# Kernel tuning notes

Measured on AMD Instinct MI355X. Metric: run time of the kernel, lower is better.

## Reference

```python
import jax, jax.numpy as jnp
import numpy as np

B, T, NT, H, L, F, NH, R = 2, 1024, 30, 1024, 8, 2816, 16, 16
HD = H // NH
LORA_SCALE = 32.0 / 16.0  # lora_alpha / r
CLAMP = 10.0
EPS = 1e-6


def _rms(x, w):
    return x * jax.lax.rsqrt(jnp.mean(x * x, axis=-1, keepdims=True) + EPS) * w


def _rope(x):
    # x: [B,T,NH,HD] -- LLaMA rotary embedding
    half = HD // 2
    inv_freq = 1.0 / (10000.0 ** (jnp.arange(0, half, dtype=jnp.float32) / half))
    ang = jnp.arange(x.shape[1], dtype=jnp.float32)[:, None] * inv_freq  # [T,half]
    cos = jnp.concatenate([jnp.cos(ang), jnp.cos(ang)], -1)[None, :, None, :]
    sin = jnp.concatenate([jnp.sin(ang), jnp.sin(ang)], -1)[None, :, None, :]
    x1, x2 = x[..., :half], x[..., half:]
    return x * cos + jnp.concatenate([-x2, x1], -1) * sin


def _lora(x, W, A, Bm):
    # W: [in,out], A: [r,in], Bm: [out,r]  (dequantized base + LoRA update)
    return x @ W + ((x @ A.T) @ Bm.T) * LORA_SCALE


def setup_inputs():
    key = jax.random.key(0)
    ks = jax.random.split(key, 16)
    n = lambda k, s, sc=0.02: jax.random.normal(k, s, jnp.float32) * sc
    return {
        'x': jax.random.normal(ks[0], (B, T, NT), jnp.float32),
        'temperature': jnp.float32(1.0),
        'state_W': n(ks[1], (NT, H), 0.1),
        'state_b': jnp.zeros((H,), jnp.float32),
        'ln1': jnp.ones((L, H), jnp.float32),
        'ln2': jnp.ones((L, H), jnp.float32),
        'Wqkv': n(ks[2], (L, 3, H, H)),
        'Aqkv': n(ks[3], (L, 3, R, H)),
        'Bqkv': n(ks[4], (L, 3, H, R)),
        'Wo': n(ks[5], (L, H, H)),
        'Ao': n(ks[6], (L, R, H)),
        'Bo': n(ks[7], (L, H, R)),
        'Wgu': n(ks[8], (L, 2, H, F)),
        'Agu': n(ks[9], (L, 2, R, H)),
        'Bgu': n(ks[10], (L, 2, F, R)),
        'Wd': n(ks[11], (L, F, H)),
        'Ad': n(ks[12], (L, R, F)),
        'Bd': n(ks[13], (L, H, R)),
        'ln_f': jnp.ones((H,), jnp.float32),
        'head_W': n(ks[14], (H, NT + 1), 0.01),
        'head_b': jnp.zeros((NT + 1,), jnp.float32),
    }


def reference(x, temperature, state_W, state_b, ln1, ln2, Wqkv, Aqkv, Bqkv,
              Wo, Ao, Bo, Wgu, Agu, Bgu, Wd, Ad, Bd, ln_f, head_W, head_b):
    causal = jnp.tril(jnp.ones((T, T), bool))

    def layer(h, p):
        l1, l2, wqkv, aqkv, bqkv, wo, ao, bo, wgu, agu, bgu, wd, ad, bd = p
        hn = _rms(h, l1)
        qkv = jnp.einsum('bth,khd->kbtd', hn, wqkv)
        qkv = qkv + jnp.einsum('kbtr,kdr->kbtd',
                               jnp.einsum('bth,krh->kbtr', hn, aqkv), bqkv) * LORA_SCALE
        q = _rope(qkv[0].reshape(B, T, NH, HD))
        k = _rope(qkv[1].reshape(B, T, NH, HD))
        v = qkv[2].reshape(B, T, NH, HD)
        scores = jnp.einsum('bqhd,bkhd->bhqk', q, k) / np.sqrt(HD).astype(np.float32)
        scores = jnp.where(causal, scores, jnp.float32(-1e9))
        probs = jax.nn.softmax(scores, axis=-1)
        att = jnp.einsum('bhqk,bkhd->bqhd', probs, v).reshape(B, T, H)
        h = h + _lora(att, wo, ao, bo)
        hn2 = _rms(h, l2)
        gu = jnp.einsum('bth,khf->kbtf', hn2, wgu)
        gu = gu + jnp.einsum('kbtr,kfr->kbtf',
                             jnp.einsum('bth,krh->kbtr', hn2, agu), bgu) * LORA_SCALE
        act = jax.nn.silu(gu[0]) * gu[1]
        h = h + _lora(act, wd, ad, bd)
        return h, None

    h = x @ state_W + state_b  # state encoder -> inputs_embeds
    h, _ = jax.lax.scan(layer, h, (ln1, ln2, Wqkv, Aqkv, Bqkv, Wo, Ao, Bo,
                                   Wgu, Agu, Bgu, Wd, Ad, Bd))
    latent = _rms(h, ln_f)  # last hidden state
    logits = latent @ head_W + head_b
    logits_clamped = jnp.clip(logits, -CLAMP, CLAMP)
    portfolio_weights = jax.nn.softmax(logits_clamped / temperature, axis=-1)
    return portfolio_weights, logits_clamped
```

## Files before the change

### kernel.cpp

```cpp
#include <hip/hip_runtime.h>
#include <hip/hip_bf16.h>
#include <cstdint>

#define B_    2
#define T_    1024
#define NT_   30
#define H_    1024
#define L_    8
#define F_    2816
#define NH_   16
#define R_    16
#define HD_   64
#define M_    2048
#define NTP1_ 31

typedef unsigned short u16;
typedef short  s16x8 __attribute__((ext_vector_type(8)));
typedef unsigned short u16x4 __attribute__((ext_vector_type(4)));
typedef unsigned short u16x8 __attribute__((ext_vector_type(8)));
typedef float  f32x4 __attribute__((ext_vector_type(4)));

__device__ __forceinline__ u16 f2bf(float f){
  __hip_bfloat16 h = __float2bfloat16(f);
  return __builtin_bit_cast(unsigned short, h);
}
__device__ __forceinline__ float bf2f(u16 u){
  uint32_t v = (uint32_t)u << 16;
  return __builtin_bit_cast(float, v);
}

__device__ __forceinline__ void async16(const void* g, void* l){
  __builtin_amdgcn_global_load_lds((const __attribute__((address_space(1))) void*)g,
                                   (__attribute__((address_space(3))) void*)l, 16, 0, 0);
}

__global__ __launch_bounds__(256, 3) void fold_kernel(
    const float* __restrict__ W, const float* __restrict__ A,
    const float* __restrict__ Bm, u16* __restrict__ Wt,
    int K, int N, long strW, long strA, long strB, long strWt)
{
  const int mat = blockIdx.z;
  W  += (long)mat * strW;  A  += (long)mat * strA;
  Bm += (long)mat * strB;  Wt += (long)mat * strWt;
  const int k0 = blockIdx.x * 64, n0 = blockIdx.y * 64;
  __shared__ float Wt_s[64][65];
  __shared__ float As[16][64];
  __shared__ float Bs[64][20];
  const int tid = threadIdx.x;
  {
    const int kr = tid >> 4;
    const int n4 = (tid & 15) * 4;
    #pragma unroll
    for (int p = 0; p < 4; p++){
      int krow = p * 16 + kr;
      float4 w = *(const float4*)(W + (long)(k0 + krow) * N + n0 + n4);
      Wt_s[n4+0][krow] = w.x; Wt_s[n4+1][krow] = w.y;
      Wt_s[n4+2][krow] = w.z; Wt_s[n4+3][krow] = w.w;
    }
    const int r = tid >> 4, kc = (tid & 15) * 4;
    *(float4*)&As[r][kc] = *(const float4*)(A + (long)r * K + k0 + kc);
    const int nb = tid >> 2, r4 = (tid & 3) * 4;
    float4 b = *(const float4*)(Bm + (long)(n0 + nb) * 16 + r4);
    Bs[nb][r4+0]=b.x; Bs[nb][r4+1]=b.y; Bs[nb][r4+2]=b.z; Bs[nb][r4+3]=b.w;
  }
  __syncthreads();
  const int ko = (tid & 7) * 8;
  const int na = tid >> 3;
  float bq0[16], bq1[16];
  #pragma unroll
  for (int c = 0; c < 4; c++){
    *(float4*)&bq0[c*4] = *(const float4*)&Bs[na][c*4];
    *(float4*)&bq1[c*4] = *(const float4*)&Bs[na+32][c*4];
  }
  float l0[8] = {}, l1[8] = {};
  #pragma unroll
  for (int r = 0; r < 16; r++){
    float a[8];
    *(float4*)&a[0] = *(const float4*)&As[r][ko];
    *(float4*)&a[4] = *(const float4*)&As[r][ko+4];
    #pragma unroll
    for (int j = 0; j < 8; j++){
      l0[j] += a[j] * bq0[r];
      l1[j] += a[j] * bq1[r];
    }
  }
  u16x8 o0, o1;
  #pragma unroll
  for (int j = 0; j < 8; j++){
    o0[j] = f2bf(Wt_s[na][ko+j]    + 2.0f * l0[j]);
    o1[j] = f2bf(Wt_s[na+32][ko+j] + 2.0f * l1[j]);
  }
  *(u16x8*)(Wt + (long)(n0+na)*K    + k0 + ko) = o0;
  *(u16x8*)(Wt + (long)(n0+na+32)*K + k0 + ko) = o1;
}

__global__ __launch_bounds__(256) void embed_kernel(
    const float* __restrict__ x, const float* __restrict__ sw,
    const float* __restrict__ sb, float* __restrict__ h)
{
  const int m = blockIdx.x;
  const float* xr = x + (long)m * NT_;
  for (int jj = threadIdx.x; jj < H_; jj += 256){
    float acc = sb[jj];
    #pragma unroll
    for (int i = 0; i < NT_; i++) acc += xr[i] * sw[i * H_ + jj];
    h[(long)m * H_ + jj] = acc;
  }
}

__global__ __launch_bounds__(256) void rms_kernel(
    float* __restrict__ hsrc, const float* __restrict__ pb,
    const float* __restrict__ w, u16* __restrict__ outp, int nparts)
{
  const int m = blockIdx.x, t = threadIdx.x;
  float4 v = ((const float4*)(hsrc + (long)m * H_))[t];
  if (nparts){
    for (int k = 0; k < nparts; k++){
      const float4 a = ((const float4*)(pb + (long)k * M_ * H_ + (long)m * H_))[t];
      v.x += a.x; v.y += a.y; v.z += a.z; v.w += a.w;
    }
    ((float4*)(hsrc + (long)m * H_))[t] = v;
  }
  float ss = v.x*v.x + v.y*v.y + v.z*v.z + v.w*v.w;
  #pragma unroll
  for (int off = 32; off >= 1; off >>= 1) ss += __shfl_xor(ss, off);
  __shared__ float red[4];
  if ((t & 63) == 0) red[t >> 6] = ss;
  __syncthreads();
  const float scale = rsqrtf((red[0]+red[1]+red[2]+red[3]) * (1.0f/H_) + 1e-6f);
  const float4 wv = ((const float4*)w)[t];
  u16x4 o;
  o[0] = f2bf(v.x*scale*wv.x); o[1] = f2bf(v.y*scale*wv.y);
  o[2] = f2bf(v.z*scale*wv.z); o[3] = f2bf(v.w*scale*wv.w);
  *(u16x4*)(outp + (long)m * H_ + t * 4) = o;
}

template<int OUTBF>
__global__ __launch_bounds__(256, 3) void gemm_bt(
    const u16* __restrict__ Ag, const u16* __restrict__ Btg, void* __restrict__ Cptr,
    int Ndim, int Kstride, int Ksteps, long zsC)
{
  const int z = blockIdx.z, Z = (int)gridDim.z;
  const int kb = Ksteps / Z, rem = Ksteps % Z;
  const int sblk = (z < rem) ? z * (kb + 1) : rem * (kb + 1) + (z - rem) * kb;
  const int klen = (kb + (z < rem ? 1 : 0)) * 64;
  Ag  += (long)sblk * 64;
  Btg += (long)sblk * 64;
  const int m0 = blockIdx.x * 128, n0 = blockIdx.y * 128;
  __shared__ alignas(16) u16 As[128 * 64];
  __shared__ alignas(16) u16 Bs[128 * 64];
  const int tid = threadIdx.x;
  const int wave = tid >> 6, lane = tid & 63;
  const int wm = (wave & 1) * 64, wn = (wave >> 1) * 64;
  const int fr = lane & 15, quad = lane >> 4;

  f32x4 acc[4][4] = {};

  for (int kt = 0; kt < klen; kt += 64){
    __syncthreads();
    #pragma unroll
    for (int c = 0; c < 4; c++){
      int lin = c * 256 + tid;
      int row = lin >> 3, p = lin & 7;
      int gc = ((p ^ (row & 7)) * 8);
      async16(Ag  + (long)(m0 + row) * Kstride + kt + gc, As + lin * 8);
      async16(Btg + (long)(n0 + row) * Kstride + kt + gc, Bs + lin * 8);
    }
    __syncthreads();
    #pragma unroll
    for (int kk = 0; kk < 2; kk++){
      s16x8 af[4], bg[4];
      #pragma unroll
      for (int i = 0; i < 4; i++){
        int rA = wm + i * 16 + fr;
        af[i] = *(const s16x8*)(As + rA * 64 + (((kk*4 + quad) ^ (rA & 7)) * 8));
        int rB = wn + i * 16 + fr;
        bg[i] = *(const s16x8*)(Bs + rB * 64 + (((kk*4 + quad) ^ (rB & 7)) * 8));
      }
      #pragma unroll
      for (int i = 0; i < 4; i++)
        #pragma unroll
        for (int j = 0; j < 4; j++)
          acc[i][j] = __builtin_amdgcn_mfma_f32_16x16x32_bf16(af[i], bg[j], acc[i][j], 0, 0, 0);
    }
  }
  #pragma unroll
  for (int i = 0; i < 4; i++){
    int row0 = m0 + wm + i * 16 + quad * 4;
    #pragma unroll
    for (int j = 0; j < 4; j++){
      int col = n0 + wn + j * 16 + fr;
      #pragma unroll
      for (int r = 0; r < 4; r++){
        long idx = (long)(row0 + r) * Ndim + col;
        if (OUTBF){
          u16* C = (u16*)Cptr + (long)blockIdx.z * zsC;
          C[idx] = f2bf(acc[i][j][r]);
        } else {
          float* C = (float*)Cptr + (long)blockIdx.z * zsC;
          C[idx] = acc[i][j][r];
        }
      }
    }
  }
}

__global__ __launch_bounds__(256, 3) void gemm_qkv(
    const u16* __restrict__ Ag, const u16* __restrict__ Btg,
    u16* __restrict__ qr, u16* __restrict__ kr, u16* __restrict__ vt)
{
  const int m0 = blockIdx.x * 128, n0 = blockIdx.y * 128;
  __shared__ alignas(16) u16 As[128 * 64];
  __shared__ alignas(16) u16 Bs[128 * 64];
  const int tid = threadIdx.x;
  const int wave = tid >> 6, lane = tid & 63;
  const int wm = (wave & 1) * 64, wn = (wave >> 1) * 64;
  const int fr = lane & 15, quad = lane >> 4;

  f32x4 acc[4][4] = {};

  for (int kt = 0; kt < H_; kt += 64){
    __syncthreads();
    #pragma unroll
    for (int c = 0; c < 4; c++){
      int lin = c * 256 + tid;
      int row = lin >> 3, p = lin & 7;
      int gc = ((p ^ (row & 7)) * 8);
      async16(Ag  + (long)(m0 + row) * H_ + kt + gc, As + lin * 8);
      async16(Btg + (long)(n0 + row) * H_ + kt + gc, Bs + lin * 8);
    }
    __syncthreads();
    #pragma unroll
    for (int kk = 0; kk < 2; kk++){
      s16x8 af[4], bg[4];
      #pragma unroll
      for (int i = 0; i < 4; i++){
        int rA = wm + i * 16 + fr;
        af[i] = *(const s16x8*)(As + rA * 64 + (((kk*4 + quad) ^ (rA & 7)) * 8));
        int rB = wn + i * 16 + fr;
        bg[i] = *(const s16x8*)(Bs + rB * 64 + (((kk*4 + quad) ^ (rB & 7)) * 8));
      }
      #pragma unroll
      for (int i = 0; i < 4; i++)
        #pragma unroll
        for (int j = 0; j < 4; j++)
          acc[i][j] = __builtin_amdgcn_mfma_f32_16x16x32_bf16(af[i], bg[j], acc[i][j], 0, 0, 0);
    }
  }
  const int sel  = n0 >> 10;
  const int nloc = (n0 & 1023) + wn;
  const int hh   = nloc >> 6;
  if (sel == 2){
    #pragma unroll
    for (int i = 0; i < 4; i++){
      int row0 = m0 + wm + i * 16 + quad * 4;
      int b = row0 >> 10, t0 = row0 & 1023;
      #pragma unroll
      for (int j = 0; j < 4; j++){
        int d = j * 16 + fr;
        u16x4 o;
        #pragma unroll
        for (int r = 0; r < 4; r++) o[r] = f2bf(acc[i][j][r]);
        *(u16x4*)(vt + ((long)((b * NH_ + hh) * HD_ + d)) * T_ + t0) = o;
      }
    }
  } else {
    u16* dst = sel ? kr : qr;
    #pragma unroll
    for (int i = 0; i < 4; i++){
      int row0 = m0 + wm + i * 16 + quad * 4;
      int b = row0 >> 10;
      #pragma unroll
      for (int j = 0; j < 2; j++){
        int d1 = j * 16 + fr;
        float freq = exp2f((float)d1 * (-13.287712379549449f / 32.0f));
        #pragma unroll
        for (int r = 0; r < 4; r++){
          int t = (row0 + r) & 1023;
          float x1 = acc[i][j][r], x2 = acc[i][j + 2][r];
          float sn, cs; __sincosf((float)t * freq, &sn, &cs);
          long base = ((long)(b * NH_ + hh) * T_ + t) * HD_;
          dst[base + d1]      = f2bf(x1 * cs - x2 * sn);
          dst[base + d1 + 32] = f2bf(x2 * cs + x1 * sn);
        }
      }
    }
  }
}

__global__ __launch_bounds__(256, 2) void gemm_gu(
    const u16* __restrict__ Ag, const u16* __restrict__ Bgw,
    const u16* __restrict__ Buw, u16* __restrict__ actb)
{
  const int m0 = blockIdx.x * 128, n0 = blockIdx.y * 128;
  __shared__ alignas(16) u16 As[128 * 64];
  __shared__ alignas(16) u16 Bg_[128 * 64];
  __shared__ alignas(16) u16 Bu_[128 * 64];
  const int tid = threadIdx.x;
  const int wave = tid >> 6, lane = tid & 63;
  const int wm = (wave & 1) * 64, wn = (wave >> 1) * 64;
  const int fr = lane & 15, quad = lane >> 4;

  f32x4 accg[4][4] = {}, accu[4][4] = {};

  for (int kt = 0; kt < H_; kt += 64){
    __syncthreads();
    #pragma unroll
    for (int c = 0; c < 4; c++){
      int lin = c * 256 + tid;
      int row = lin >> 3, p = lin & 7;
      int gc = ((p ^ (row & 7)) * 8);
      async16(Ag  + (long)(m0 + row) * H_ + kt + gc, As  + lin * 8);
      async16(Bgw + (long)(n0 + row) * H_ + kt + gc, Bg_ + lin * 8);
      async16(Buw + (long)(n0 + row) * H_ + kt + gc, Bu_ + lin * 8);
    }
    __syncthreads();
    #pragma unroll
    for (int kk = 0; kk < 2; kk++){
      s16x8 af[4], bb[4];
      #pragma unroll
      for (int i = 0; i < 4; i++){
        int rA = wm + i * 16 + fr;
        af[i] = *(const s16x8*)(As + rA * 64 + (((kk*4 + quad) ^ (rA & 7)) * 8));
      }
      #pragma unroll
      for (int i = 0; i < 4; i++){
        int rB = wn + i * 16 + fr;
        bb[i] = *(const s16x8*)(Bg_ + rB * 64 + (((kk*4 + quad) ^ (rB & 7)) * 8));
      }
      #pragma unroll
      for (int i = 0; i < 4; i++)
        #pragma unroll
        for (int j = 0; j < 4; j++)
          accg[i][j] = __builtin_amdgcn_mfma_f32_16x16x32_bf16(af[i], bb[j], accg[i][j], 0, 0, 0);
      #pragma unroll
      for (int i = 0; i < 4; i++){
        int rB = wn + i * 16 + fr;
        bb[i] = *(const s16x8*)(Bu_ + rB * 64 + (((kk*4 + quad) ^ (rB & 7)) * 8));
      }
      #pragma unroll
      for (int i = 0; i < 4; i++)
        #pragma unroll
        for (int j = 0; j < 4; j++)
          accu[i][j] = __builtin_amdgcn_mfma_f32_16x16x32_bf16(af[i], bb[j], accu[i][j], 0, 0, 0);
    }
  }
  #pragma unroll
  for (int i = 0; i < 4; i++){
    int row0 = m0 + wm + i * 16 + quad * 4;
    #pragma unroll
    for (int j = 0; j < 4; j++){
      int col = n0 + wn + j * 16 + fr;
      #pragma unroll
      for (int r = 0; r < 4; r++){
        float g = accg[i][j][r], u = accu[i][j][r];
        float act = g / (1.0f + __expf(-g)) * u;
        actb[(long)(row0 + r) * F_ + col] = f2bf(act);
      }
    }
  }
}

__global__ __launch_bounds__(256, 2) void attn_kernel(
    const u16* __restrict__ qr, const u16* __restrict__ kr,
    const u16* __restrict__ vt, u16* __restrict__ att)
{
  const int bh = blockIdx.y;
  const int b = bh >> 4, hh = bh & 15;
  __shared__ alignas(16) u16 Qs[64 * 64];
  __shared__ alignas(16) u16 Ks[128 * 64];
  __shared__ alignas(16) u16 Vs[64 * 128];
  __shared__ alignas(16) u16 Ps[64 * 136];
  const int tid = threadIdx.x;
  const int wave = tid >> 6, lane = tid & 63, fr = lane & 15, quad = lane >> 4;
  const int wrow = wave * 16;
  const u16* kgb = kr + (long)bh * T_ * HD_;
  const u16* vgb = vt + (long)bh * HD_ * T_;

  for (int pass = 0; pass < 2; pass++){
    const int qt = pass ? (15 - (int)blockIdx.x) : (int)blockIdx.x;
    __syncthreads();
    const u16* qg = qr + ((long)bh * T_ + qt * 64) * HD_;
    #pragma unroll
    for (int c = 0; c < 2; c++){
      int lin = c * 256 + tid, row = lin >> 3, p = lin & 7;
      async16(qg + row * HD_ + ((p ^ (row & 7)) * 8), Qs + lin * 8);
    }
    f32x4 o_acc[4] = {};
    float m_r[4] = {-1e30f, -1e30f, -1e30f, -1e30f};
    float l_r[4] = {};
    const int kmax = (qt * 64 + 63) >> 7;

    for (int kt = 0; kt <= kmax; kt++){
      __syncthreads();
      const u16* kg = kgb + (long)kt * 128 * HD_;
      #pragma unroll
      for (int c = 0; c < 4; c++){
        int lin = c * 256 + tid, row = lin >> 3, p = lin & 7;
        async16(kg + row * HD_ + ((p ^ (row & 7)) * 8), Ks + lin * 8);
      }
      #pragma unroll
      for (int c = 0; c < 4; c++){
        int lin = c * 256 + tid, row = lin >> 4, p = lin & 15;
        async16(vgb + (long)row * T_ + kt * 128 + ((p ^ (row & 15)) * 8), Vs + lin * 8);
      }
      __syncthreads();

      f32x4 s[8] = {};
      s16x8 aq[2];
      {
        int rA = wrow + fr;
        #pragma unroll
        for (int kk = 0; kk < 2; kk++)
          aq[kk] = *(const s16x8*)(Qs + rA * 64 + (((kk*4 + quad) ^ (rA & 7)) * 8));
      }
      #pragma unroll
      for (int ik = 0; ik < 8; ik++){
        #pragma unroll
        for (int kk = 0; kk < 2; kk++){
          int rB = ik * 16 + fr;
          s16x8 bk = *(const s16x8*)(Ks + rB * 64 + (((kk*4 + quad) ^ (rB & 7)) * 8));
          s[ik] = __builtin_amdgcn_mfma_f32_16x16x32_bf16(aq[kk], bk, s[ik], 0, 0, 0);
        }
      }
      const bool diag = (kt == kmax);
      #pragma unroll
      for (int r = 0; r < 4; r++){
        const int qgi = qt * 64 + wrow + quad * 4 + r;
        float tmax = -1e30f;
        #pragma unroll
        for (int ik = 0; ik < 8; ik++){
          float v = s[ik][r] * 0.125f;
          if (diag && (kt * 128 + ik * 16 + fr) > qgi) v = -1e9f;
          s[ik][r] = v;
          tmax = fmaxf(tmax, v);
        }
        #pragma unroll
        for (int off = 8; off >= 1; off >>= 1) tmax = fmaxf(tmax, __shfl_xor(tmax, off));
        const float mnew = fmaxf(m_r[r], tmax);
        const float alpha = __expf(m_r[r] - mnew);
        m_r[r] = mnew;
        float ts = 0.0f;
        const int prow = wrow + quad * 4 + r;
        #pragma unroll
        for (int ik = 0; ik < 8; ik++){
          float p = __expf(s[ik][r] - mnew);
          ts += p;
          Ps[prow * 136 + ik * 16 + fr] = f2bf(p);
        }
        #pragma unroll
        for (int off = 8; off >= 1; off >>= 1) ts += __shfl_xor(ts, off);
        l_r[r] = l_r[r] * alpha + ts;
        #pragma unroll
        for (int jd = 0; jd < 4; jd++) o_acc[jd][r] *= alpha;
      }
      #pragma unroll
      for (int kk2 = 0; kk2 < 4; kk2++){
        s16x8 ap = *(const s16x8*)(Ps + (wrow + fr) * 136 + kk2 * 32 + quad * 8);
        #pragma unroll
        for (int jd = 0; jd < 4; jd++){
          int rV = jd * 16 + fr;
          s16x8 bv = *(const s16x8*)(Vs + rV * 128 + (((kk2*4 + quad) ^ (rV & 15)) * 8));
          o_acc[jd] = __builtin_amdgcn_mfma_f32_16x16x32_bf16(ap, bv, o_acc[jd], 0, 0, 0);
        }
      }
    }
    #pragma unroll
    for (int r = 0; r < 4; r++){
      const int t_loc = qt * 64 + wrow + quad * 4 + r;
      const long rowbase = ((long)b * T_ + t_loc) * H_ + hh * HD_;
      const float inv = 1.0f / l_r[r];
      #pragma unroll
      for (int jd = 0; jd < 4; jd++)
        att[rowbase + jd * 16 + fr] = f2bf(o_acc[jd][r] * inv);
    }
  }
}

__global__ __launch_bounds__(256) void head_kernel(
    const float* __restrict__ hsrc, const float* __restrict__ pb,
    const float* __restrict__ lnf, const float* __restrict__ hw, const float* __restrict__ hb,
    const float* __restrict__ temp, float* __restrict__ outp)
{
  const int m = blockIdx.x, t = threadIdx.x;
  __shared__ float lat[H_];
  __shared__ float red[4];
  __shared__ float part[8][32];
  float4 v = ((const float4*)(hsrc + (long)m * H_))[t];
  #pragma unroll
  for (int k = 0; k < 4; k++){
    const float4 a = ((const float4*)(pb + (long)k * M_ * H_ + (long)m * H_))[t];
    v.x += a.x; v.y += a.y; v.z += a.z; v.w += a.w;
  }
  float ss = v.x*v.x + v.y*v.y + v.z*v.z + v.w*v.w;
  #pragma unroll
  for (int off = 32; off >= 1; off >>= 1) ss += __shfl_xor(ss, off);
  if ((t & 63) == 0) red[t >> 6] = ss;
  __syncthreads();
  const float scale = rsqrtf((red[0]+red[1]+red[2]+red[3]) * (1.0f/H_) + 1e-6f);
  const float4 wv = ((const float4*)lnf)[t];
  lat[t*4+0] = v.x*scale*wv.x;  lat[t*4+1] = v.y*scale*wv.y;
  lat[t*4+2] = v.z*scale*wv.z;  lat[t*4+3] = v.w*scale*wv.w;
  __syncthreads();
  const int j = t & 31, seg = t >> 5;
  float pp = 0.0f;
  if (j < 31){
    const float* wp = hw + j;
    for (int k = seg * 128; k < seg * 128 + 128; k++) pp += lat[k] * wp[(long)k * 31];
  }
  part[seg][j] = pp;
  __syncthreads();
  if (t < 32){
    float dot = 0.0f;
    #pragma unroll
    for (int s2 = 0; s2 < 8; s2++) dot += part[s2][t];
    const float logit = (t < 31) ? dot + hb[t] : -1e30f;
    const float lc = fminf(fmaxf(logit, -10.0f), 10.0f);
    const float z = (t < 31) ? lc / temp[0] : -1e30f;
    float mx = z;
    #pragma unroll
    for (int off = 16; off >= 1; off >>= 1) mx = fmaxf(mx, __shfl_xor(mx, off, 32));
    const float e = (t < 31) ? __expf(z - mx) : 0.0f;
    float sum = e;
    #pragma unroll
    for (int off = 16; off >= 1; off >>= 1) sum += __shfl_xor(sum, off, 32);
    if (t < 31){
      outp[(long)m * NTP1_ + t] = e / sum;
      outp[(long)M_ * NTP1_ + (long)m * NTP1_ + t] = lc;
    }
  }
}

extern "C" void kernel_launch(void* const* d_in, const int* in_sizes, int n_in,
                              void* d_out, int out_size, void* d_ws, size_t ws_size,
                              hipStream_t stream) {
  const float* x    = (const float*)d_in[0];
  const float* temp = (const float*)d_in[1];
  const float* sW   = (const float*)d_in[2];
  const float* sb   = (const float*)d_in[3];
  const float* ln1  = (const float*)d_in[4];
  const float* ln2  = (const float*)d_in[5];
  const float* Wqkv = (const float*)d_in[6];
  const float* Aqkv = (const float*)d_in[7];
  const float* Bqkv = (const float*)d_in[8];
  const float* Wo   = (const float*)d_in[9];
  const float* Ao   = (const float*)d_in[10];
  const float* Bo   = (const float*)d_in[11];
  const float* Wgu  = (const float*)d_in[12];
  const float* Agu  = (const float*)d_in[13];
  const float* Bgu  = (const float*)d_in[14];
  const float* Wd   = (const float*)d_in[15];
  const float* Ad   = (const float*)d_in[16];
  const float* Bd   = (const float*)d_in[17];
  const float* lnf  = (const float*)d_in[18];
  const float* hW   = (const float*)d_in[19];
  const float* hb   = (const float*)d_in[20];
  float* out = (float*)d_out;

  uint8_t* ws = (uint8_t*)d_ws;
  size_t off = 0;
  auto alloc = [&](size_t bytes) -> void* {
    void* p = ws + off;
    off += (bytes + 255) & ~(size_t)255;
    return p;
  };
  u16*   wt_qkv = (u16*)  alloc((size_t)L_ * 3 * H_ * H_ * 2);
  u16*   wt_o   = (u16*)  alloc((size_t)L_ * H_ * H_ * 2);
  u16*   wt_gu  = (u16*)  alloc((size_t)L_ * 2 * F_ * H_ * 2);
  u16*   wt_d   = (u16*)  alloc((size_t)L_ * H_ * F_ * 2);
  float* h      = (float*)alloc((size_t)M_ * H_ * 4);
  u16*   hn     = (u16*)  alloc((size_t)M_ * H_ * 2);
  float* p0     = (float*)alloc((size_t)4 * M_ * H_ * 4);
  u16*   qr     = (u16*)  alloc((size_t)M_ * H_ * 2);
  u16*   krr    = (u16*)  alloc((size_t)M_ * H_ * 2);
  u16*   vtb    = (u16*)  alloc((size_t)M_ * H_ * 2);
  u16*   attb   = (u16*)  alloc((size_t)M_ * H_ * 2);
  u16*   actb   = (u16*)  alloc((size_t)M_ * F_ * 2);

  fold_kernel<<<dim3(16, 16, L_ * 3), 256, 0, stream>>>(Wqkv, Aqkv, Bqkv, wt_qkv,
      H_, H_, (long)H_ * H_, (long)R_ * H_, (long)H_ * R_, (long)H_ * H_);
  fold_kernel<<<dim3(16, 16, L_), 256, 0, stream>>>(Wo, Ao, Bo, wt_o,
      H_, H_, (long)H_ * H_, (long)R_ * H_, (long)H_ * R_, (long)H_ * H_);
  fold_kernel<<<dim3(16, 44, L_ * 2), 256, 0, stream>>>(Wgu, Agu, Bgu, wt_gu,
      H_, F_, (long)H_ * F_, (long)R_ * H_, (long)F_ * R_, (long)F_ * H_);
  fold_kernel<<<dim3(44, 16, L_), 256, 0, stream>>>(Wd, Ad, Bd, wt_d,
      F_, H_, (long)F_ * H_, (long)R_ * F_, (long)H_ * R_, (long)H_ * F_);

  embed_kernel<<<M_, 256, 0, stream>>>(x, sW, sb, h);

  for (int l = 0; l < L_; l++){
    rms_kernel<<<M_, 256, 0, stream>>>(h, p0, ln1 + (long)l * H_, hn, l > 0 ? 4 : 0);
    gemm_qkv<<<dim3(16, 24), 256, 0, stream>>>(hn, wt_qkv + (long)l * 3 * H_ * H_,
        qr, krr, vtb);
    attn_kernel<<<dim3(8, B_ * NH_), 256, 0, stream>>>(qr, krr, vtb, attb);
    gemm_bt<0><<<dim3(16, 8, 2), 256, 0, stream>>>(attb, wt_o + (long)l * H_ * H_,
        p0, H_, H_, 16, (long)M_ * H_);
    rms_kernel<<<M_, 256, 0, stream>>>(h, p0, ln2 + (long)l * H_, hn, 2);
    gemm_gu<<<dim3(16, 22), 256, 0, stream>>>(hn,
        wt_gu + (long)l * 2 * F_ * H_, wt_gu + (long)l * 2 * F_ * H_ + (long)F_ * H_, actb);
    gemm_bt<0><<<dim3(16, 8, 4), 256, 0, stream>>>(actb, wt_d + (long)l * H_ * F_,
        p0, H_, F_, 44, (long)M_ * H_);
  }

  head_kernel<<<M_, 256, 0, stream>>>(h, p0, lnf, hW, hb, temp, out);
}
```

Measured before the change: 1.590 ms.

## Store split-K partials in bf16, shrink gate-up tiles, and simplify attention grid

Split-K partial sums from the output and down projections are now written as bf16 instead of fp32, and the RMS and head kernels read them that way. This halves partial-buffer traffic but adds rounding error to the residual update. The gate/up GEMM uses 128x64 tiles with 3 blocks per CU to fill the machine better. Attention drops its two-pass paired-tile scheme and launches one block per query tile, which doubles the grid but leaves the causal load imbalance to the hardware scheduler.

```diff
diff --git a/kernel.cpp b/kernel.cpp
--- a/kernel.cpp
+++ b/kernel.cpp
@@ -109,15 +109,15 @@
 }
 
 __global__ __launch_bounds__(256) void rms_kernel(
-    float* __restrict__ hsrc, const float* __restrict__ pb,
+    float* __restrict__ hsrc, const u16* __restrict__ pb,
     const float* __restrict__ w, u16* __restrict__ outp, int nparts)
 {
   const int m = blockIdx.x, t = threadIdx.x;
   float4 v = ((const float4*)(hsrc + (long)m * H_))[t];
   if (nparts){
     for (int k = 0; k < nparts; k++){
-      const float4 a = ((const float4*)(pb + (long)k * M_ * H_ + (long)m * H_))[t];
-      v.x += a.x; v.y += a.y; v.z += a.z; v.w += a.w;
+      u16x4 a = *(const u16x4*)(pb + (long)k * M_ * H_ + (long)m * H_ + t * 4);
+      v.x += bf2f(a[0]); v.y += bf2f(a[1]); v.z += bf2f(a[2]); v.w += bf2f(a[3]);
     }
     ((float4*)(hsrc + (long)m * H_))[t] = v;
   }
@@ -288,20 +288,20 @@
   }
 }
 
-__global__ __launch_bounds__(256, 2) void gemm_gu(
+__global__ __launch_bounds__(256, 3) void gemm_gu(
     const u16* __restrict__ Ag, const u16* __restrict__ Bgw,
     const u16* __restrict__ Buw, u16* __restrict__ actb)
 {
-  const int m0 = blockIdx.x * 128, n0 = blockIdx.y * 128;
+  const int m0 = blockIdx.x * 128, n0 = blockIdx.y * 64;
   __shared__ alignas(16) u16 As[128 * 64];
-  __shared__ alignas(16) u16 Bg_[128 * 64];
-  __shared__ alignas(16) u16 Bu_[128 * 64];
+  __shared__ alignas(16) u16 Bg_[64 * 64];
+  __shared__ alignas(16) u16 Bu_[64 * 64];
   const int tid = threadIdx.x;
   const int wave = tid >> 6, lane = tid & 63;
-  const int wm = (wave & 1) * 64, wn = (wave >> 1) * 64;
+  const int wm = (wave & 1) * 64, wn = (wave >> 1) * 32;
   const int fr = lane & 15, quad = lane >> 4;
 
-  f32x4 accg[4][4] = {}, accu[4][4] = {};
+  f32x4 accg[4][2] = {}, accu[4][2] = {};
 
   for (int kt = 0; kt < H_; kt += 64){
     __syncthreads();
@@ -309,47 +309,45 @@
     for (int c = 0; c < 4; c++){
       int lin = c * 256 + tid;
       int row = lin >> 3, p = lin & 7;
+      async16(Ag + (long)(m0 + row) * H_ + kt + ((p ^ (row & 7)) * 8), As + lin * 8);
+    }
+    #pragma unroll
+    for (int c = 0; c < 2; c++){
+      int lin = c * 256 + tid;
+      int row = lin >> 3, p = lin & 7;
       int gc = ((p ^ (row & 7)) * 8);
-      async16(Ag  + (long)(m0 + row) * H_ + kt + gc, As  + lin * 8);
       async16(Bgw + (long)(n0 + row) * H_ + kt + gc, Bg_ + lin * 8);
       async16(Buw + (long)(n0 + row) * H_ + kt + gc, Bu_ + lin * 8);
     }
     __syncthreads();
     #pragma unroll
     for (int kk = 0; kk < 2; kk++){
-      s16x8 af[4], bb[4];
+      s16x8 af[4], bg[2], bu[2];
       #pragma unroll
       for (int i = 0; i < 4; i++){
         int rA = wm + i * 16 + fr;
         af[i] = *(const s16x8*)(As + rA * 64 + (((kk*4 + quad) ^ (rA & 7)) * 8));
       }
       #pragma unroll
-      for (int i = 0; i < 4; i++){
-        int rB = wn + i * 16 + fr;
-        bb[i] = *(const s16x8*)(Bg_ + rB * 64 + (((kk*4 + quad) ^ (rB & 7)) * 8));
+      for (int j = 0; j < 2; j++){
+        int rB = wn + j * 16 + fr;
+        bg[j] = *(const s16x8*)(Bg_ + rB * 64 + (((kk*4 + quad) ^ (rB & 7)) * 8));
+        bu[j] = *(const s16x8*)(Bu_ + rB * 64 + (((kk*4 + quad) ^ (rB & 7)) * 8));
       }
       #pragma unroll
       for (int i = 0; i < 4; i++)
         #pragma unroll
-        for (int j = 0; j < 4; j++)
-          accg[i][j] = __builtin_amdgcn_mfma_f32_16x16x32_bf16(af[i], bb[j], accg[i][j], 0, 0, 0);
-      #pragma unroll
-      for (int i = 0; i < 4; i++){
-        int rB = wn + i * 16 + fr;
-        bb[i] = *(const s16x8*)(Bu_ + rB * 64 + (((kk*4 + quad) ^ (rB & 7)) * 8));
-      }
-      #pragma unroll
-      for (int i = 0; i < 4; i++)
-        #pragma unroll
-        for (int j = 0; j < 4; j++)
-          accu[i][j] = __builtin_amdgcn_mfma_f32_16x16x32_bf16(af[i], bb[j], accu[i][j], 0, 0, 0);
+        for (int j = 0; j < 2; j++){
+          accg[i][j] = __builtin_amdgcn_mfma_f32_16x16x32_bf16(af[i], bg[j], accg[i][j], 0, 0, 0);
+          accu[i][j] = __builtin_amdgcn_mfma_f32_16x16x32_bf16(af[i], bu[j], accu[i][j], 0, 0, 0);
+        }
     }
   }
   #pragma unroll
   for (int i = 0; i < 4; i++){
     int row0 = m0 + wm + i * 16 + quad * 4;
     #pragma unroll
-    for (int j = 0; j < 4; j++){
+    for (int j = 0; j < 2; j++){
       int col = n0 + wn + j * 16 + fr;
       #pragma unroll
       for (int r = 0; r < 4; r++){
@@ -367,6 +365,7 @@
 {
   const int bh = blockIdx.y;
   const int b = bh >> 4, hh = bh & 15;
+  const int qt = blockIdx.x;
   __shared__ alignas(16) u16 Qs[64 * 64];
   __shared__ alignas(16) u16 Ks[128 * 64];
   __shared__ alignas(16) u16 Vs[64 * 128];
@@ -377,108 +376,104 @@
   const u16* kgb = kr + (long)bh * T_ * HD_;
   const u16* vgb = vt + (long)bh * HD_ * T_;
 
-  for (int pass = 0; pass < 2; pass++){
-    const int qt = pass ? (15 - (int)blockIdx.x) : (int)blockIdx.x;
-    __syncthreads();
-    const u16* qg = qr + ((long)bh * T_ + qt * 64) * HD_;
-    #pragma unroll
-    for (int c = 0; c < 2; c++){
+  const u16* qg = qr + ((long)bh * T_ + qt * 64) * HD_;
+  #pragma unroll
+  for (int c = 0; c < 2; c++){
+    int lin = c * 256 + tid, row = lin >> 3, p = lin & 7;
+    async16(qg + row * HD_ + ((p ^ (row & 7)) * 8), Qs + lin * 8);
+  }
+  f32x4 o_acc[4] = {};
+  float m_r[4] = {-1e30f, -1e30f, -1e30f, -1e30f};
+  float l_r[4] = {};
+  const int kmax = (qt * 64 + 63) >> 7;
+
+  for (int kt = 0; kt <= kmax; kt++){
+    __syncthreads();
+    const u16* kg = kgb + (long)kt * 128 * HD_;
+    #pragma unroll
+    for (int c = 0; c < 4; c++){
       int lin = c * 256 + tid, row = lin >> 3, p = lin & 7;
-      async16(qg + row * HD_ + ((p ^ (row & 7)) * 8), Qs + lin * 8);
-    }
-    f32x4 o_acc[4] = {};
-    float m_r[4] = {-1e30f, -1e30f, -1e30f, -1e30f};
-    float l_r[4] = {};
-    const int kmax = (qt * 64 + 63) >> 7;
-
-    for (int kt = 0; kt <= kmax; kt++){
-      __syncthreads();
-      const u16* kg = kgb + (long)kt * 128 * HD_;
-      #pragma unroll
-      for (int c = 0; c < 4; c++){
-        int lin = c * 256 + tid, row = lin >> 3, p = lin & 7;
-        async16(kg + row * HD_ + ((p ^ (row & 7)) * 8), Ks + lin * 8);
-      }
-      #pragma unroll
-      for (int c = 0; c < 4; c++){
-        int lin = c * 256 + tid, row = lin >> 4, p = lin & 15;
-        async16(vgb + (long)row * T_ + kt * 128 + ((p ^ (row & 15)) * 8), Vs + lin * 8);
-      }
-      __syncthreads();
-
-      f32x4 s[8] = {};
-      s16x8 aq[2];
-      {
-        int rA = wrow + fr;
-        #pragma unroll
-        for (int kk = 0; kk < 2; kk++)
-          aq[kk] = *(const s16x8*)(Qs + rA * 64 + (((kk*4 + quad) ^ (rA & 7)) * 8));
-      }
+      async16(kg + row * HD_ + ((p ^ (row & 7)) * 8), Ks + lin * 8);
+    }
+    #pragma unroll
+    for (int c = 0; c < 4; c++){
+      int lin = c * 256 + tid, row = lin >> 4, p = lin & 15;
+      async16(vgb + (long)row * T_ + kt * 128 + ((p ^ (row & 15)) * 8), Vs + lin * 8);
+    }
+    __syncthreads();
+
+    f32x4 s[8] = {};
+    s16x8 aq[2];
+    {
+      int rA = wrow + fr;
+      #pragma unroll
+      for (int kk = 0; kk < 2; kk++)
+        aq[kk] = *(const s16x8*)(Qs + rA * 64 + (((kk*4 + quad) ^ (rA & 7)) * 8));
+    }
+    #pragma unroll
+    for (int ik = 0; ik < 8; ik++){
+      #pragma unroll
+      for (int kk = 0; kk < 2; kk++){
+        int rB = ik * 16 + fr;
+        s16x8 bk = *(const s16x8*)(Ks + rB * 64 + (((kk*4 + quad) ^ (rB & 7)) * 8));
+        s[ik] = __builtin_amdgcn_mfma_f32_16x16x32_bf16(aq[kk], bk, s[ik], 0, 0, 0);
+      }
+    }
+    const bool diag = (kt == kmax);
+    #pragma unroll
+    for (int r = 0; r < 4; r++){
+      const int qgi = qt * 64 + wrow + quad * 4 + r;
+      float tmax = -1e30f;
       #pragma unroll
       for (int ik = 0; ik < 8; ik++){
-        #pragma unroll
-        for (int kk = 0; kk < 2; kk++){
-          int rB = ik * 16 + fr;
-          s16x8 bk = *(const s16x8*)(Ks + rB * 64 + (((kk*4 + quad) ^ (rB & 7)) * 8));
-          s[ik] = __builtin_amdgcn_mfma_f32_16x16x32_bf16(aq[kk], bk, s[ik], 0, 0, 0);
-        }
-      }
-      const bool diag = (kt == kmax);
-      #pragma unroll
-      for (int r = 0; r < 4; r++){
-        const int qgi = qt * 64 + wrow + quad * 4 + r;
-        float tmax = -1e30f;
-        #pragma unroll
-        for (int ik = 0; ik < 8; ik++){
-          float v = s[ik][r] * 0.125f;
-          if (diag && (kt * 128 + ik * 16 + fr) > qgi) v = -1e9f;
-          s[ik][r] = v;
-          tmax = fmaxf(tmax, v);
-        }
-        #pragma unroll
-        for (int off = 8; off >= 1; off >>= 1) tmax = fmaxf(tmax, __shfl_xor(tmax, off));
-        const float mnew = fmaxf(m_r[r], tmax);
-        const float alpha = __expf(m_r[r] - mnew);
-        m_r[r] = mnew;
-        float ts = 0.0f;
-        const int prow = wrow + quad * 4 + r;
-        #pragma unroll
-        for (int ik = 0; ik < 8; ik++){
-          float p = __expf(s[ik][r] - mnew);
-          ts += p;
-          Ps[prow * 136 + ik * 16 + fr] = f2bf(p);
-        }
-        #pragma unroll
-        for (int off = 8; off >= 1; off >>= 1) ts += __shfl_xor(ts, off);
-        l_r[r] = l_r[r] * alpha + ts;
-        #pragma unroll
-        for (int jd = 0; jd < 4; jd++) o_acc[jd][r] *= alpha;
-      }
-      #pragma unroll
-      for (int kk2 = 0; kk2 < 4; kk2++){
-        s16x8 ap = *(const s16x8*)(Ps + (wrow + fr) * 136 + kk2 * 32 + quad * 8);
-        #pragma unroll
-        for (int jd = 0; jd < 4; jd++){
-          int rV = jd * 16 + fr;
-          s16x8 bv = *(const s16x8*)(Vs + rV * 128 + (((kk2*4 + quad) ^ (rV & 15)) * 8));
-          o_acc[jd] = __builtin_amdgcn_mfma_f32_16x16x32_bf16(ap, bv, o_acc[jd], 0, 0, 0);
-        }
-      }
-    }
-    #pragma unroll
-    for (int r = 0; r < 4; r++){
-      const int t_loc = qt * 64 + wrow + quad * 4 + r;
-      const long rowbase = ((long)b * T_ + t_loc) * H_ + hh * HD_;
-      const float inv = 1.0f / l_r[r];
-      #pragma unroll
-      for (int jd = 0; jd < 4; jd++)
-        att[rowbase + jd * 16 + fr] = f2bf(o_acc[jd][r] * inv);
-    }
+        float v = s[ik][r] * 0.125f;
+        if (diag && (kt * 128 + ik * 16 + fr) > qgi) v = -1e9f;
+        s[ik][r] = v;
+        tmax = fmaxf(tmax, v);
+      }
+      #pragma unroll
+      for (int off = 8; off >= 1; off >>= 1) tmax = fmaxf(tmax, __shfl_xor(tmax, off));
+      const float mnew = fmaxf(m_r[r], tmax);
+      const float alpha = __expf(m_r[r] - mnew);
+      m_r[r] = mnew;
+      float ts = 0.0f;
+      const int prow = wrow + quad * 4 + r;
+      #pragma unroll
+      for (int ik = 0; ik < 8; ik++){
+        float p = __expf(s[ik][r] - mnew);
+        ts += p;
+        Ps[prow * 136 + ik * 16 + fr] = f2bf(p);
+      }
+      #pragma unroll
+      for (int off = 8; off >= 1; off >>= 1) ts += __shfl_xor(ts, off);
+      l_r[r] = l_r[r] * alpha + ts;
+      #pragma unroll
+      for (int jd = 0; jd < 4; jd++) o_acc[jd][r] *= alpha;
+    }
+    #pragma unroll
+    for (int kk2 = 0; kk2 < 4; kk2++){
+      s16x8 ap = *(const s16x8*)(Ps + (wrow + fr) * 136 + kk2 * 32 + quad * 8);
+      #pragma unroll
+      for (int jd = 0; jd < 4; jd++){
+        int rV = jd * 16 + fr;
+        s16x8 bv = *(const s16x8*)(Vs + rV * 128 + (((kk2*4 + quad) ^ (rV & 15)) * 8));
+        o_acc[jd] = __builtin_amdgcn_mfma_f32_16x16x32_bf16(ap, bv, o_acc[jd], 0, 0, 0);
+      }
+    }
+  }
+  #pragma unroll
+  for (int r = 0; r < 4; r++){
+    const int t_loc = qt * 64 + wrow + quad * 4 + r;
+    const long rowbase = ((long)b * T_ + t_loc) * H_ + hh * HD_;
+    const float inv = 1.0f / l_r[r];
+    #pragma unroll
+    for (int jd = 0; jd < 4; jd++)
+      att[rowbase + jd * 16 + fr] = f2bf(o_acc[jd][r] * inv);
   }
 }
 
 __global__ __launch_bounds__(256) void head_kernel(
-    const float* __restrict__ hsrc, const float* __restrict__ pb,
+    const float* __restrict__ hsrc, const u16* __restrict__ pb,
     const float* __restrict__ lnf, const float* __restrict__ hw, const float* __restrict__ hb,
     const float* __restrict__ temp, float* __restrict__ outp)
 {
@@ -489,8 +484,8 @@
   float4 v = ((const float4*)(hsrc + (long)m * H_))[t];
   #pragma unroll
   for (int k = 0; k < 4; k++){
-    const float4 a = ((const float4*)(pb + (long)k * M_ * H_ + (long)m * H_))[t];
-    v.x += a.x; v.y += a.y; v.z += a.z; v.w += a.w;
+    u16x4 a = *(const u16x4*)(pb + (long)k * M_ * H_ + (long)m * H_ + t * 4);
+    v.x += bf2f(a[0]); v.y += bf2f(a[1]); v.z += bf2f(a[2]); v.w += bf2f(a[3]);
   }
   float ss = v.x*v.x + v.y*v.y + v.z*v.z + v.w*v.w;
   #pragma unroll
@@ -570,7 +565,7 @@
   u16*   wt_d   = (u16*)  alloc((size_t)L_ * H_ * F_ * 2);
   float* h      = (float*)alloc((size_t)M_ * H_ * 4);
   u16*   hn     = (u16*)  alloc((size_t)M_ * H_ * 2);
-  float* p0     = (float*)alloc((size_t)4 * M_ * H_ * 4);
+  u16*   pb16   = (u16*)  alloc((size_t)4 * M_ * H_ * 2);
   u16*   qr     = (u16*)  alloc((size_t)M_ * H_ * 2);
   u16*   krr    = (u16*)  alloc((size_t)M_ * H_ * 2);
   u16*   vtb    = (u16*)  alloc((size_t)M_ * H_ * 2);
@@ -589,18 +584,18 @@
   embed_kernel<<<M_, 256, 0, stream>>>(x, sW, sb, h);
 
   for (int l = 0; l < L_; l++){
-    rms_kernel<<<M_, 256, 0, stream>>>(h, p0, ln1 + (long)l * H_, hn, l > 0 ? 4 : 0);
+    rms_kernel<<<M_, 256, 0, stream>>>(h, pb16, ln1 + (long)l * H_, hn, l > 0 ? 4 : 0);
     gemm_qkv<<<dim3(16, 24), 256, 0, stream>>>(hn, wt_qkv + (long)l * 3 * H_ * H_,
         qr, krr, vtb);
-    attn_kernel<<<dim3(8, B_ * NH_), 256, 0, stream>>>(qr, krr, vtb, attb);
-    gemm_bt<0><<<dim3(16, 8, 2), 256, 0, stream>>>(attb, wt_o + (long)l * H_ * H_,
-        p0, H_, H_, 16, (long)M_ * H_);
-    rms_kernel<<<M_, 256, 0, stream>>>(h, p0, ln2 + (long)l * H_, hn, 2);
-    gemm_gu<<<dim3(16, 22), 256, 0, stream>>>(hn,
+    attn_kernel<<<dim3(16, B_ * NH_), 256, 0, stream>>>(qr, krr, vtb, attb);
+    gemm_bt<1><<<dim3(16, 8, 2), 256, 0, stream>>>(attb, wt_o + (long)l * H_ * H_,
+        pb16, H_, H_, 16, (long)M_ * H_);
+    rms_kernel<<<M_, 256, 0, stream>>>(h, pb16, ln2 + (long)l * H_, hn, 2);
+    gemm_gu<<<dim3(16, 44), 256, 0, stream>>>(hn,
         wt_gu + (long)l * 2 * F_ * H_, wt_gu + (long)l * 2 * F_ * H_ + (long)F_ * H_, actb);
-    gemm_bt<0><<<dim3(16, 8, 4), 256, 0, stream>>>(actb, wt_d + (long)l * H_ * F_,
-        p0, H_, F_, 44, (long)M_ * H_);
-  }
-
-  head_kernel<<<M_, 256, 0, stream>>>(h, p0, lnf, hW, hb, temp, out);
-}
+    gemm_bt<1><<<dim3(16, 8, 4), 256, 0, stream>>>(actb, wt_d + (long)l * H_ * F_,
+        pb16, H_, F_, 44, (long)M_ * H_);
+  }
+
+  head_kernel<<<M_, 256, 0, stream>>>(h, pb16, lnf, hW, hb, temp, out);
+}
```

New measurement: 1.554 ms. -2.3%, faster.
